# Kernel tuning notes

Hardware: AMD Instinct MI355X
Metric: run time of the kernel (lower is better)

Reference implementation:

```python
import jax, jax.numpy as jnp
import numpy as np

B, S, D, H, FF = 2, 2048, 1024, 16, 4096
HD = D // H
EPS = 1e-5


def _ln(x, g, b):
    m = jnp.mean(x, axis=-1, keepdims=True)
    v = jnp.mean((x - m) ** 2, axis=-1, keepdims=True)
    return (x - m) * jax.lax.rsqrt(v + EPS) * g + b


def _rope(x, cos, sin):
    # non-standard RoPE: split full d_model at half, rotate (pre head-split)
    half = x.shape[-1] // 2
    x1, x2 = x[..., :half], x[..., half:]
    return jnp.concatenate([x1 * cos - x2 * sin, x1 * sin + x2 * cos], axis=-1)


def _heads(x, b, s):
    return x.reshape(b, s, H, HD).transpose(0, 2, 1, 3)  # [b,h,s,hd]


def _attn(q, k, v):
    scores = jnp.einsum('bhqd,bhkd->bhqk', q, k) / jnp.sqrt(jnp.float32(HD))
    w = jax.nn.softmax(scores, axis=-1)
    return jnp.einsum('bhqk,bhkd->bhqd', w, v)


def setup_inputs() -> dict:
    key = jax.random.key(0)
    ks = jax.random.split(key, 32)
    sc = 0.02
    d = {
        'x': jax.random.normal(ks[0], (B, S, D), jnp.float32),
        'cond_emb': jax.random.normal(ks[1], (B, D), jnp.float32),
    }
    # proper RoPE tables over half_dim = D//2
    pos = np.arange(S)[:, None]
    inv = 1.0 / (10000.0 ** (np.arange(D // 2) / (D // 2)))
    ang = pos * inv[None, :]
    d['cos_pos'] = jnp.asarray(np.cos(ang), jnp.float32)
    d['sin_pos'] = jnp.asarray(np.sin(ang), jnp.float32)
    names = ['Wq', 'Wk', 'Wv', 'Wo', 'Wqc', 'Wkc', 'Wvc', 'Woc']
    for i, n in enumerate(names):
        d[n] = jax.random.normal(ks[2 + i], (D, D), jnp.float32) * sc
        d['b' + n[1:]] = jnp.zeros((D,), jnp.float32)
    d['W1'] = jax.random.normal(ks[12], (D, FF), jnp.float32) * sc
    d['b1'] = jnp.zeros((FF,), jnp.float32)
    d['W2'] = jax.random.normal(ks[13], (FF, D), jnp.float32) * sc
    d['b2'] = jnp.zeros((D,), jnp.float32)
    for i in (1, 2, 3):
        d[f'g{i}'] = jnp.ones((D,), jnp.float32)
        d[f'be{i}'] = jnp.zeros((D,), jnp.float32)
    return d


def reference(x, cond_emb, cos_pos, sin_pos,
              Wq, bq, Wk, bk, Wv, bv, Wo, bo,
              Wqc, bqc, Wkc, bkc, Wvc, bvc, Woc, boc,
              W1, b1, W2, b2, g1, be1, g2, be2, g3, be3):
    b, s, _ = x.shape
    # self-attention with RoPE applied on full d_model before head split
    residual = x
    xn = _ln(x, g1, be1)
    q = _rope(xn @ Wq + bq, cos_pos, sin_pos)
    k = _rope(xn @ Wk + bk, cos_pos, sin_pos)
    v = xn @ Wv + bv
    o = _attn(_heads(q, b, s), _heads(k, b, s), _heads(v, b, s))
    o = o.transpose(0, 2, 1, 3).reshape(b, s, D) @ Wo + bo
    x = residual + o
    # cross-attention with single-token context
    residual = x
    xn = _ln(x, g2, be2)
    cond = cond_emb[:, None, :]  # [b,1,D]
    qc = _heads(xn @ Wqc + bqc, b, s)
    kc = _heads(cond @ Wkc + bkc, b, 1)
    vc = _heads(cond @ Wvc + bvc, b, 1)
    oc = _attn(qc, kc, vc)
    oc = oc.transpose(0, 2, 1, 3).reshape(b, s, D) @ Woc + boc
    x = residual + oc
    # FFN (exact GELU)
    residual = x
    xn = _ln(x, g3, be3)
    h = jax.nn.gelu(xn @ W1 + b1, approximate=False)
    return residual + (h @ W2 + b2)
```

## Files before the change

### kernel.cpp

```cpp
#include <hip/hip_runtime.h>
#include <cmath>

#define B_  2
#define S_  2048
#define D_  1024
#define H_  16
#define HD_ 64
#define FF_ 4096
#define M_  4096

typedef __attribute__((ext_vector_type(8))) __bf16 bf16x8;
typedef __attribute__((ext_vector_type(4))) __bf16 bf16x4;
typedef __attribute__((ext_vector_type(4))) float  f32x4;

__device__ __forceinline__ void gload_lds16(void* lds, const void* g) {
    __builtin_amdgcn_global_load_lds(
        (const __attribute__((address_space(1))) unsigned int*)g,
        (__attribute__((address_space(3))) unsigned int*)lds,
        16, 0, 0);
}

#define FENCE() asm volatile("" ::: "memory")

__global__ __launch_bounds__(256)
void tcast(const float* __restrict__ src, __bf16* __restrict__ dst, int K, int N)
{
    __shared__ float t[32][33];
    int tx = threadIdx.x & 31, ty = threadIdx.x >> 5;
    int k0 = blockIdx.y * 32, n0 = blockIdx.x * 32;
#pragma unroll
    for (int i = 0; i < 4; ++i)
        t[ty + i * 8][tx] = src[(size_t)(k0 + ty + i * 8) * N + n0 + tx];
    __syncthreads();
#pragma unroll
    for (int i = 0; i < 4; ++i)
        dst[(size_t)(n0 + ty + i * 8) * K + k0 + tx] = (__bf16)t[tx][ty + i * 8];
}

__global__ __launch_bounds__(256)
void tcast3(const float* __restrict__ wa, const float* __restrict__ wb,
            const float* __restrict__ wc, __bf16* __restrict__ dstb)
{
    __shared__ float t[32][33];
    const float* src = blockIdx.z == 0 ? wa : (blockIdx.z == 1 ? wb : wc);
    __bf16* dst = dstb + (size_t)blockIdx.z * 1024 * 1024;
    int tx = threadIdx.x & 31, ty = threadIdx.x >> 5;
    int k0 = blockIdx.y * 32, n0 = blockIdx.x * 32;
#pragma unroll
    for (int i = 0; i < 4; ++i)
        t[ty + i * 8][tx] = src[(size_t)(k0 + ty + i * 8) * 1024 + n0 + tx];
    __syncthreads();
#pragma unroll
    for (int i = 0; i < 4; ++i)
        dst[(size_t)(n0 + ty + i * 8) * 1024 + k0 + tx] = (__bf16)t[tx][ty + i * 8];
}

__global__ __launch_bounds__(256)
void catb(const float* __restrict__ a, const float* __restrict__ b,
          const float* __restrict__ c, float* __restrict__ o)
{
    int i = blockIdx.x * 256 + threadIdx.x;
    o[i] = i < 1024 ? a[i] : (i < 2048 ? b[i - 1024] : c[i - 2048]);
}

__global__ __launch_bounds__(256)
void colgemv(const float* __restrict__ inp, const float* __restrict__ W,
             const float* __restrict__ bias, float* __restrict__ out, int K, int N)
{
    __shared__ float part[4][16];
    const int b = blockIdx.y;
    const int t = threadIdx.x;
    const int w = t >> 6, lane = t & 63;
    const int colIdx = lane & 15;
    const int col = blockIdx.x * 16 + colIdx;
    const int ks = w * 4 + (lane >> 4);
    const int kpt = K >> 4;
    const float* ip = inp + (size_t)b * K + ks * kpt;
    const float* wp = W + (size_t)ks * kpt * N + col;
    float acc = 0.f;
#pragma unroll 8
    for (int i = 0; i < kpt; ++i)
        acc += ip[i] * wp[(size_t)i * N];
    acc += __shfl_xor(acc, 16);
    acc += __shfl_xor(acc, 32);
    if (lane < 16) part[w][colIdx] = acc;
    __syncthreads();
    if (t < 16) {
        float r = part[0][t] + part[1][t] + part[2][t] + part[3][t]
                + bias[blockIdx.x * 16 + t];
        out[(size_t)b * N + blockIdx.x * 16 + t] = r;
    }
}

__global__ __launch_bounds__(256)
void ln_cast(const float* __restrict__ x, const float* __restrict__ g,
             const float* __restrict__ be, __bf16* __restrict__ out)
{
    int row = blockIdx.x, tid = threadIdx.x;
    const float4* xp = (const float4*)(x + (size_t)row * D_);
    float4 v = xp[tid];
    float s  = v.x + v.y + v.z + v.w;
    float s2 = v.x * v.x + v.y * v.y + v.z * v.z + v.w * v.w;
#pragma unroll
    for (int off = 32; off > 0; off >>= 1) {
        s  += __shfl_down(s, off);
        s2 += __shfl_down(s2, off);
    }
    __shared__ float rs[4], rs2[4];
    int wid = tid >> 6, lane = tid & 63;
    if (lane == 0) { rs[wid] = s; rs2[wid] = s2; }
    __syncthreads();
    float tot  = rs[0] + rs[1] + rs[2] + rs[3];
    float tot2 = rs2[0] + rs2[1] + rs2[2] + rs2[3];
    float mean = tot * (1.0f / D_);
    float var  = tot2 * (1.0f / D_) - mean * mean;
    float rstd = rsqrtf(var + 1e-5f);
    float4 gv = ((const float4*)g)[tid];
    float4 bv = ((const float4*)be)[tid];
    bf16x4 ov;
    ov[0] = (__bf16)((v.x - mean) * rstd * gv.x + bv.x);
    ov[1] = (__bf16)((v.y - mean) * rstd * gv.y + bv.y);
    ov[2] = (__bf16)((v.z - mean) * rstd * gv.z + bv.z);
    ov[3] = (__bf16)((v.w - mean) * rstd * gv.w + bv.w);
    ((bf16x4*)(out + (size_t)row * D_))[tid] = ov;
}

__global__ __launch_bounds__(128)
void rope_qk(const __bf16* __restrict__ qkv, const float* __restrict__ cosp,
             const float* __restrict__ sinp, __bf16* __restrict__ Qh,
             __bf16* __restrict__ Kh)
{
    int row = blockIdx.x, tid = threadIdx.x;
    int b = row >> 11, s = row & 2047;
    float4 c  = ((const float4*)(cosp + (size_t)s * 512))[tid];
    float4 sn = ((const float4*)(sinp + (size_t)s * 512))[tid];
    int d0 = tid * 4;
    int h1 = d0 >> 6, dd = d0 & 63;
#pragma unroll
    for (int which = 0; which < 2; ++which) {
        const int off = which * 1024;
        const float scale = which ? 1.0f : 0.18033688f;
        __bf16* out = which ? Kh : Qh;
        bf16x4 a  = *(const bf16x4*)(qkv + (size_t)row * 3072 + off + tid * 4);
        bf16x4 bb = *(const bf16x4*)(qkv + (size_t)row * 3072 + off + 512 + tid * 4);
        float x1a = (float)a[0],  x1b = (float)a[1],  x1c = (float)a[2],  x1d = (float)a[3];
        float x2a = (float)bb[0], x2b = (float)bb[1], x2c = (float)bb[2], x2d = (float)bb[3];
        bf16x4 o1, o2;
        o1[0] = (__bf16)((x1a * c.x - x2a * sn.x) * scale);
        o1[1] = (__bf16)((x1b * c.y - x2b * sn.y) * scale);
        o1[2] = (__bf16)((x1c * c.z - x2c * sn.z) * scale);
        o1[3] = (__bf16)((x1d * c.w - x2d * sn.w) * scale);
        o2[0] = (__bf16)((x1a * sn.x + x2a * c.x) * scale);
        o2[1] = (__bf16)((x1b * sn.y + x2b * c.y) * scale);
        o2[2] = (__bf16)((x1c * sn.z + x2c * c.z) * scale);
        o2[3] = (__bf16)((x1d * sn.w + x2d * c.w) * scale);
        *(bf16x4*)(out + ((size_t)((b * H_ + h1) * S_ + s) * HD_) + dd) = o1;
        *(bf16x4*)(out + ((size_t)((b * H_ + h1 + 8) * S_ + s) * HD_) + dd) = o2;
    }
}

__global__ __launch_bounds__(256)
void vtrans2(const __bf16* __restrict__ qkv, __bf16* __restrict__ Vt)
{
    __shared__ __bf16 t[32][33];
    int tx = threadIdx.x & 31, ty = threadIdx.x >> 5;
    int bh = blockIdx.z;
    int b = bh >> 4, h = bh & 15;
    int s0 = blockIdx.y * 32, d0 = blockIdx.x * 32;
    __bf16* dst = Vt + (size_t)bh * HD_ * S_;
#pragma unroll
    for (int i = 0; i < 4; ++i)
        t[ty + i * 8][tx] = qkv[(size_t)(b * 2048 + s0 + ty + i * 8) * 3072
                                + 2048 + h * 64 + d0 + tx];
    __syncthreads();
#pragma unroll
    for (int i = 0; i < 4; ++i)
        dst[(size_t)(d0 + ty + i * 8) * S_ + s0 + tx] = t[tx][ty + i * 8];
}

template<int EPI>
__global__ __launch_bounds__(512)
void gemm8(const __bf16* __restrict__ A, const __bf16* __restrict__ Bt,
           const float* __restrict__ bias, __bf16* __restrict__ o0,
           __bf16* __restrict__ o1, int M, int N, int K, int klen)
{
    __shared__ __align__(16) char smem[131072];
    const int tid = threadIdx.x;
    const int wid = tid >> 6, lane = tid & 63;
    const int l15 = lane & 15, l16 = lane >> 4;
    const int wm = wid >> 2, wn = wid & 3;

    const int gx = gridDim.x;
    const int nwg = gx * gridDim.y;
    int wg = blockIdx.y * gx + blockIdx.x;
    wg = (wg & 7) * (nwg >> 3) + (wg >> 3);
    const int n0 = (wg % gx) * 256;
    const int m0 = (wg / gx) * 256;
    const int kz = blockIdx.z * klen;
    const size_t K2 = (size_t)K * 2;

    const int srow = tid >> 3;
    const int scol = ((tid & 7) * 16) ^ ((srow & 7) << 4);
    const char* gA = (const char*)A + (size_t)(m0 + srow) * K2 + (size_t)kz * 2 + scol;
    const char* gB = (const char*)Bt + (size_t)(n0 + srow) * K2 + (size_t)kz * 2 + scol;

    auto stageA = [&](int c) {
        char* d = (char*)smem + c * 32768 + wid * 1024;
        gload_lds16(d,         gA);
        gload_lds16(d + 8192,  gA + 64 * K2);
        gload_lds16(d + 16384, gA + 128 * K2);
        gload_lds16(d + 24576, gA + 192 * K2);
    };
    auto stageB = [&](int c) {
        char* d = (char*)smem + 65536 + c * 32768 + wid * 1024;
        gload_lds16(d,         gB);
        gload_lds16(d + 8192,  gB + 64 * K2);
        gload_lds16(d + 16384, gB + 128 * K2);
        gload_lds16(d + 24576, gB + 192 * K2);
    };

    const int sw = (l15 & 7) << 4;
    const int x0 = (l16 * 16) ^ sw;
    const int x1 = (64 + l16 * 16) ^ sw;
    const int aoff = (wm * 128 + l15) * 128;
    const int boff = 65536 + (wn * 64 + l15) * 128;

    f32x4 acc[8][4] = {};
    const int NT = klen >> 6;

    stageA(0); stageB(0); gA += 128; gB += 128;
    stageA(1); stageB(1); gA += 128; gB += 128;
    asm volatile("s_waitcnt vmcnt(8)" ::: "memory");
    __builtin_amdgcn_s_barrier();

    for (int t = 0; t < NT; ++t) {
        const int cur = t & 1;
        const char* sa = (const char*)smem + cur * 32768;
        const bool pf = (t + 2) < NT;

        bf16x8 af0[8], af1[8];
        bf16x8 b00, b01, b02, b03, b10, b11, b12, b13;

#pragma unroll
        for (int mi = 0; mi < 8; ++mi)
            af0[mi] = *(const bf16x8*)(sa + aoff + mi * 2048 + x0);
        b00 = *(const bf16x8*)(sa + boff + 0 * 2048 + x0);
        b01 = *(const bf16x8*)(sa + boff + 1 * 2048 + x0);
        FENCE();
        __builtin_amdgcn_s_barrier();
        __builtin_amdgcn_s_setprio(1);
#pragma unroll
        for (int mi = 0; mi < 8; ++mi) {
            acc[mi][0] = __builtin_amdgcn_mfma_f32_16x16x32_bf16(af0[mi], b00, acc[mi][0], 0, 0, 0);
            acc[mi][1] = __builtin_amdgcn_mfma_f32_16x16x32_bf16(af0[mi], b01, acc[mi][1], 0, 0, 0);
        }
        __builtin_amdgcn_s_setprio(0);

#pragma unroll
        for (int mi = 0; mi < 8; ++mi)
            af1[mi] = *(const bf16x8*)(sa + aoff + mi * 2048 + x1);
        b02 = *(const bf16x8*)(sa + boff + 2 * 2048 + x0);
        b03 = *(const bf16x8*)(sa + boff + 3 * 2048 + x0);
        FENCE();
        __builtin_amdgcn_s_barrier();
        __builtin_amdgcn_s_setprio(1);
#pragma unroll
        for (int mi = 0; mi < 8; ++mi) {
            acc[mi][2] = __builtin_amdgcn_mfma_f32_16x16x32_bf16(af0[mi], b02, acc[mi][2], 0, 0, 0);
            acc[mi][3] = __builtin_amdgcn_mfma_f32_16x16x32_bf16(af0[mi], b03, acc[mi][3], 0, 0, 0);
        }
        __builtin_amdgcn_s_setprio(0);

        b10 = *(const bf16x8*)(sa + boff + 0 * 2048 + x1);
        b11 = *(const bf16x8*)(sa + boff + 1 * 2048 + x1);
        FENCE();
        __builtin_amdgcn_s_barrier();
        if (pf) stageA(cur);
        __builtin_amdgcn_s_setprio(1);
#pragma unroll
        for (int mi = 0; mi < 8; ++mi) {
            acc[mi][0] = __builtin_amdgcn_mfma_f32_16x16x32_bf16(af1[mi], b10, acc[mi][0], 0, 0, 0);
            acc[mi][1] = __builtin_amdgcn_mfma_f32_16x16x32_bf16(af1[mi], b11, acc[mi][1], 0, 0, 0);
        }
        __builtin_amdgcn_s_setprio(0);

        b12 = *(const bf16x8*)(sa + boff + 2 * 2048 + x1);
        b13 = *(const bf16x8*)(sa + boff + 3 * 2048 + x1);
        FENCE();
        __builtin_amdgcn_s_barrier();
        if (pf) { stageB(cur); gA += 128; gB += 128; }
        __builtin_amdgcn_s_setprio(1);
#pragma unroll
        for (int mi = 0; mi < 8; ++mi) {
            acc[mi][2] = __builtin_amdgcn_mfma_f32_16x16x32_bf16(af1[mi], b12, acc[mi][2], 0, 0, 0);
            acc[mi][3] = __builtin_amdgcn_mfma_f32_16x16x32_bf16(af1[mi], b13, acc[mi][3], 0, 0, 0);
        }
        __builtin_amdgcn_s_setprio(0);
        if (pf) asm volatile("s_waitcnt vmcnt(8)" ::: "memory");
        else    asm volatile("s_waitcnt vmcnt(0)" ::: "memory");
        __builtin_amdgcn_s_barrier();
        FENCE();
    }

#pragma unroll
    for (int mi = 0; mi < 8; ++mi)
#pragma unroll
        for (int ni = 0; ni < 4; ++ni) {
            int gc = n0 + wn * 64 + ni * 16 + l15;
            float bb = (EPI == 2) ? 0.f : bias[gc];
#pragma unroll
            for (int r = 0; r < 4; ++r) {
                int gr = m0 + wm * 128 + mi * 16 + l16 * 4 + r;
                float v = acc[mi][ni][r] + bb;
                if constexpr (EPI == 0) {
                    o0[(size_t)gr * N + gc] = (__bf16)v;
                } else if constexpr (EPI == 1) {
                    o0[(size_t)gr * N + gc] =
                        (__bf16)(0.5f * v * (1.0f + erff(v * 0.70710678118f)));
                } else {
                    const size_t PSZ = (size_t)M_ * 1024;
                    __bf16* po = (blockIdx.z < 2) ? (o0 + blockIdx.z * PSZ)
                                                  : (o1 + (blockIdx.z - 2) * PSZ);
                    po[(size_t)gr * N + gc] = (__bf16)v;
                }
            }
        }
}

__global__ __launch_bounds__(256)
void ffn2_red(const __bf16* __restrict__ pA, const __bf16* __restrict__ pB,
              const float* __restrict__ x2, const float* __restrict__ b2,
              float* __restrict__ out)
{
    const size_t PSZ = (size_t)M_ * 1024;
    size_t i = ((size_t)blockIdx.x * 256 + threadIdx.x) * 8;
    bf16x8 a0 = *(const bf16x8*)(pA + i);
    bf16x8 a1 = *(const bf16x8*)(pA + PSZ + i);
    bf16x8 c0 = *(const bf16x8*)(pB + i);
    bf16x8 c1 = *(const bf16x8*)(pB + PSZ + i);
    float4 xa = *(const float4*)(x2 + i);
    float4 xb = *(const float4*)(x2 + i + 4);
    float xs[8] = {xa.x, xa.y, xa.z, xa.w, xb.x, xb.y, xb.z, xb.w};
#pragma unroll
    for (int j = 0; j < 8; ++j) {
        int col = (int)((i + j) & 1023);
        out[i + j] = xs[j] + b2[col]
                   + (float)a0[j] + (float)a1[j] + (float)c0[j] + (float)c1[j];
    }
}

__global__ __launch_bounds__(256)
void gemm_bt(const __bf16* __restrict__ A, const __bf16* __restrict__ Bt,
             const float* __restrict__ bias, const float* __restrict__ resid,
             const float* __restrict__ extra, float* __restrict__ outF,
             int M, int N, int K)
{
    __shared__ __align__(16) __bf16 As[128 * 64];
    __shared__ __align__(16) __bf16 Bs[128 * 64];
    const int tid = threadIdx.x;
    const int wid = tid >> 6, lane = tid & 63;
    const int m0 = blockIdx.y * 128, n0 = blockIdx.x * 128;
    const int wm = wid >> 1, wn = wid & 1;
    const int l15 = lane & 15, l16 = lane >> 4;

    f32x4 acc[4][4] = {};
    char* asb = (char*)As;
    char* bsb = (char*)Bs;
    const char* ag = (const char*)A;
    const char* bg = (const char*)Bt;
    const int srow = lane >> 3;
    const int scolsw = ((lane & 7) * 16) ^ (srow << 4);

    for (int k0 = 0; k0 < K; k0 += 64) {
        __syncthreads();
#pragma unroll
        for (int i = 0; i < 4; ++i) {
            int j = wid * 4 + i;
            int row = j * 8 + srow;
            gload_lds16(asb + j * 1024,
                        ag + (size_t)(m0 + row) * (K * 2) + k0 * 2 + scolsw);
        }
#pragma unroll
        for (int i = 0; i < 4; ++i) {
            int j = wid * 4 + i;
            int row = j * 8 + srow;
            gload_lds16(bsb + j * 1024,
                        bg + (size_t)(n0 + row) * (K * 2) + k0 * 2 + scolsw);
        }
        __syncthreads();

        bf16x8 af[4][2], bfr[4][2];
#pragma unroll
        for (int mi = 0; mi < 4; ++mi) {
            int row = wm * 64 + mi * 16 + l15;
            int swl = (row & 7) << 4;
#pragma unroll
            for (int kk = 0; kk < 2; ++kk)
                af[mi][kk] = *(const bf16x8*)(asb + row * 128 + ((l16 * 16 + kk * 64) ^ swl));
        }
#pragma unroll
        for (int ni = 0; ni < 4; ++ni) {
            int row = wn * 64 + ni * 16 + l15;
            int swl = (row & 7) << 4;
#pragma unroll
            for (int kk = 0; kk < 2; ++kk)
                bfr[ni][kk] = *(const bf16x8*)(bsb + row * 128 + ((l16 * 16 + kk * 64) ^ swl));
        }
#pragma unroll
        for (int mi = 0; mi < 4; ++mi)
#pragma unroll
            for (int ni = 0; ni < 4; ++ni) {
                acc[mi][ni] = __builtin_amdgcn_mfma_f32_16x16x32_bf16(af[mi][0], bfr[ni][0], acc[mi][ni], 0, 0, 0);
                acc[mi][ni] = __builtin_amdgcn_mfma_f32_16x16x32_bf16(af[mi][1], bfr[ni][1], acc[mi][ni], 0, 0, 0);
            }
    }

#pragma unroll
    for (int mi = 0; mi < 4; ++mi)
#pragma unroll
        for (int ni = 0; ni < 4; ++ni) {
            int gc = n0 + wn * 64 + ni * 16 + l15;
            float bb = bias[gc];
#pragma unroll
            for (int r = 0; r < 4; ++r) {
                int gr = m0 + wm * 64 + mi * 16 + l16 * 4 + r;
                float v = acc[mi][ni][r] + bb;
                size_t idx = (size_t)gr * N + gc;
                int b = gr >> 11;
                outF[idx] = resid[idx] + v + extra[(size_t)b * N + gc];
            }
        }
}

__global__ __launch_bounds__(512)
void attn_fwd(const __bf16* __restrict__ Qh, const __bf16* __restrict__ Kh,
              const __bf16* __restrict__ Vt, __bf16* __restrict__ Op,
              float* __restrict__ Lp)
{
    __shared__ __align__(16) char smem[49152];
    const int tid = threadIdx.x, wid = tid >> 6, lane = tid & 63;
    const int l15 = lane & 15, l16 = lane >> 4;

    const int wg = blockIdx.x;
    const int rr = wg >> 3;
    const int qb = rr & 15;
    const int split = (rr >> 4) & 1;
    const int bh = (wg & 7) + 8 * (rr >> 5);
    const int kt0 = split * 16;

    const int q0 = qb * 128 + wid * 16;
    const size_t qkbase = (size_t)bh * S_ * HD_;

    bf16x8 qf[2];
    {
        const __bf16* qp = Qh + qkbase + (size_t)(q0 + l15) * HD_ + l16 * 8;
        qf[0] = *(const bf16x8*)qp;
        qf[1] = *(const bf16x8*)(qp + 32);
    }
    f32x4 o[4] = {};
    f32x4 accs = {};
    bf16x8 ones;
#pragma unroll
    for (int j = 0; j < 8; ++j) ones[j] = (__bf16)1.0f;

    const int srow = lane >> 3;
    const int scolsw = ((lane & 7) * 16) ^ ((srow & 7) << 4);
    const char* kg = (const char*)(Kh + qkbase);
    const char* vg = (const char*)(Vt + (size_t)bh * HD_ * S_);

    auto stage = [&](int c, int t) {
        int s0 = t * 64;
        int row = wid * 8 + srow;
        gload_lds16(smem + c * 8192 + wid * 1024,
                    kg + (size_t)(s0 + row) * 128 + scolsw);
        gload_lds16(smem + 16384 + c * 8192 + wid * 1024,
                    vg + (size_t)row * (S_ * 2) + s0 * 2 + scolsw);
    };

    const int NT = 16;
    stage(0, kt0);
    stage(1, kt0 + 1);
    asm volatile("s_waitcnt vmcnt(2)" ::: "memory");
    __builtin_amdgcn_s_barrier();

    for (int ki = 0; ki < NT; ++ki) {
        const int cur = ki & 1;
        const char* Kl = smem + cur * 8192;
        const char* Vl = smem + 16384 + cur * 8192;
        char* Pl = smem + 32768 + wid * 2048;

        f32x4 st[4];
        __builtin_amdgcn_s_setprio(1);
#pragma unroll
        for (int t = 0; t < 4; ++t) {
            int row = t * 16 + l15;
            int swl = (row & 7) << 4;
            bf16x8 ak0 = *(const bf16x8*)(Kl + row * 128 + ((l16 * 16) ^ swl));
            bf16x8 ak1 = *(const bf16x8*)(Kl + row * 128 + ((l16 * 16 + 64) ^ swl));
            f32x4 z = {0.f, 0.f, 0.f, 0.f};
            z = __builtin_amdgcn_mfma_f32_16x16x32_bf16(ak0, qf[0], z, 0, 0, 0);
            st[t] = __builtin_amdgcn_mfma_f32_16x16x32_bf16(ak1, qf[1], z, 0, 0, 0);
        }
        __builtin_amdgcn_s_setprio(0);

        float p[4][4];
#pragma unroll
        for (int t = 0; t < 4; ++t)
#pragma unroll
            for (int r = 0; r < 4; ++r) p[t][r] = exp2f(st[t][r]);

        {
            char* pw = Pl + l15 * 128;
            int swl = (l15 & 7) << 4;
#pragma unroll
            for (int t = 0; t < 4; ++t) {
                bf16x4 pk;
                pk[0] = (__bf16)p[t][0]; pk[1] = (__bf16)p[t][1];
                pk[2] = (__bf16)p[t][2]; pk[3] = (__bf16)p[t][3];
                *(bf16x4*)(pw + ((t * 32 + l16 * 8) ^ swl)) = pk;
            }
        }
        {
            const char* pr = Pl + l15 * 128;
            int swp = (l15 & 7) << 4;
            bf16x8 ap0 = *(const bf16x8*)(pr + ((l16 * 16) ^ swp));
            bf16x8 ap1 = *(const bf16x8*)(pr + ((l16 * 16 + 64) ^ swp));
            __builtin_amdgcn_s_setprio(1);
            accs = __builtin_amdgcn_mfma_f32_16x16x32_bf16(ap0, ones, accs, 0, 0, 0);
            accs = __builtin_amdgcn_mfma_f32_16x16x32_bf16(ap1, ones, accs, 0, 0, 0);
#pragma unroll
            for (int dg = 0; dg < 4; ++dg) {
                int row = dg * 16 + l15;
                int swl = (row & 7) << 4;
                bf16x8 bv0 = *(const bf16x8*)(Vl + row * 128 + ((l16 * 16) ^ swl));
                bf16x8 bv1 = *(const bf16x8*)(Vl + row * 128 + ((l16 * 16 + 64) ^ swl));
                o[dg] = __builtin_amdgcn_mfma_f32_16x16x32_bf16(ap0, bv0, o[dg], 0, 0, 0);
                o[dg] = __builtin_amdgcn_mfma_f32_16x16x32_bf16(ap1, bv1, o[dg], 0, 0, 0);
            }
            __builtin_amdgcn_s_setprio(0);
        }

        FENCE();
        __builtin_amdgcn_s_barrier();
        if (ki + 2 < NT) {
            stage(cur, kt0 + ki + 2);
            asm volatile("s_waitcnt vmcnt(2)" ::: "memory");
        } else {
            asm volatile("s_waitcnt vmcnt(0)" ::: "memory");
        }
        __builtin_amdgcn_s_barrier();
        FENCE();
    }

    __bf16* ob = Op + ((size_t)split * 65536 + (size_t)bh * 2048) * 64;
#pragma unroll
    for (int r = 0; r < 4; ++r) {
        float inv = 1.0f / accs[r];
        int qg = q0 + l16 * 4 + r;
#pragma unroll
        for (int dg = 0; dg < 4; ++dg)
            ob[(size_t)qg * 64 + dg * 16 + l15] = (__bf16)(o[dg][r] * inv);
    }
    if (l15 == 0) {
#pragma unroll
        for (int r = 0; r < 4; ++r)
            Lp[(size_t)split * 65536 + (size_t)bh * 2048 + q0 + l16 * 4 + r]
                = log2f(accs[r]);
    }
}

__global__ __launch_bounds__(256)
void attn_merge(const __bf16* __restrict__ Op, const float* __restrict__ Lp,
                __bf16* __restrict__ O)
{
    int idx = blockIdx.x * 256 + threadIdx.x;
    int bh = idx >> 14;
    int rem = idx & 16383;
    int s = rem >> 3;
    int d0 = (rem & 7) * 8;
    size_t qi = (size_t)bh * 2048 + s;
    float L1 = Lp[qi], L2 = Lp[65536 + qi];
    float Lm = fmaxf(L1, L2);
    float w1 = exp2f(L1 - Lm), w2 = exp2f(L2 - Lm);
    float inv = 1.0f / (w1 + w2);
    w1 *= inv; w2 *= inv;
    bf16x8 o1 = *(const bf16x8*)(Op + qi * 64 + d0);
    bf16x8 o2 = *(const bf16x8*)(Op + (size_t)65536 * 64 + qi * 64 + d0);
    int b = bh >> 4, h = bh & 15;
    __bf16* op = O + ((size_t)(b * S_ + s) * D_) + h * 64 + d0;
    bf16x8 ov;
#pragma unroll
    for (int j = 0; j < 8; ++j)
        ov[j] = (__bf16)(w1 * (float)o1[j] + w2 * (float)o2[j]);
    *(bf16x8*)op = ov;
}

extern "C" void kernel_launch(void* const* d_in, const int* in_sizes, int n_in,
                              void* d_out, int out_size, void* d_ws, size_t ws_size,
                              hipStream_t stream)
{
    (void)in_sizes; (void)n_in; (void)out_size; (void)ws_size;
    const float* x    = (const float*)d_in[0];
    const float* cond = (const float*)d_in[1];
    const float* cosp = (const float*)d_in[2];
    const float* sinp = (const float*)d_in[3];
    const float* Wq = (const float*)d_in[4];  const float* bq = (const float*)d_in[5];
    const float* Wk = (const float*)d_in[6];  const float* bk = (const float*)d_in[7];
    const float* Wv = (const float*)d_in[8];  const float* bv = (const float*)d_in[9];
    const float* Wo = (const float*)d_in[10]; const float* bo = (const float*)d_in[11];
    const float* Wvc = (const float*)d_in[16]; const float* bvc = (const float*)d_in[17];
    const float* Woc = (const float*)d_in[18]; const float* boc = (const float*)d_in[19];
    const float* W1 = (const float*)d_in[20]; const float* b1 = (const float*)d_in[21];
    const float* W2 = (const float*)d_in[22]; const float* b2 = (const float*)d_in[23];
    const float* g1 = (const float*)d_in[24]; const float* be1 = (const float*)d_in[25];
    const float* g3 = (const float*)d_in[28]; const float* be3 = (const float*)d_in[29];

    char* ws = (char*)d_ws;
    const size_t MB = 1ull << 20;
    __bf16* WqkvT = (__bf16*)(ws + 0 * MB);
    __bf16* WoT   = (__bf16*)(ws + 6 * MB);
    __bf16* W1T   = (__bf16*)(ws + 8 * MB);
    __bf16* W2T   = (__bf16*)(ws + 16 * MB);
    __bf16* xn    = (__bf16*)(ws + 24 * MB);
    __bf16* qkvh  = (__bf16*)(ws + 32 * MB);
    __bf16* Qh    = (__bf16*)(ws + 56 * MB);
    __bf16* Kh    = (__bf16*)(ws + 64 * MB);
    __bf16* Vt    = (__bf16*)(ws + 72 * MB);
    __bf16* oflat = (__bf16*)(ws + 80 * MB);
    float*  bqkv  = (float*)(ws + 88 * MB);
    float*  vc    = (float*)(ws + 88 * MB + 16384);
    float*  ocp   = (float*)(ws + 88 * MB + 32768);
    __bf16* Opart = (__bf16*)(ws + 32 * MB);
    float*  Lpart = (float*)(ws + 48 * MB);
    float*  x2    = (float*)(ws + 32 * MB);
    __bf16* hbuf  = (__bf16*)(ws + 48 * MB);
    __bf16* pA    = (__bf16*)(ws + 0 * MB);
    __bf16* pB    = (__bf16*)(ws + 80 * MB);

    tcast3<<<dim3(32, 32, 3), 256, 0, stream>>>(Wq, Wk, Wv, WqkvT);
    tcast<<<dim3(32, 32),  256, 0, stream>>>(Wo, WoT, 1024, 1024);
    tcast<<<dim3(128, 32), 256, 0, stream>>>(W1, W1T, 1024, 4096);
    tcast<<<dim3(32, 128), 256, 0, stream>>>(W2, W2T, 4096, 1024);
    catb<<<12, 256, 0, stream>>>(bq, bk, bv, bqkv);
    colgemv<<<dim3(64, 2), 256, 0, stream>>>(cond, Wvc, bvc, vc, 1024, 1024);
    colgemv<<<dim3(64, 2), 256, 0, stream>>>(vc, Woc, boc, ocp, 1024, 1024);
    ln_cast<<<M_, 256, 0, stream>>>(x, g1, be1, xn);
    gemm8<0><<<dim3(12, 16, 1), 512, 0, stream>>>(xn, WqkvT, bqkv, qkvh, nullptr,
                                                  M_, 3072, 1024, 1024);
    rope_qk<<<M_, 128, 0, stream>>>(qkvh, cosp, sinp, Qh, Kh);
    vtrans2<<<dim3(2, 64, 32), 256, 0, stream>>>(qkvh, Vt);
    attn_fwd<<<1024, 512, 0, stream>>>(Qh, Kh, Vt, Opart, Lpart);
    attn_merge<<<2048, 256, 0, stream>>>(Opart, Lpart, oflat);
    gemm_bt<<<dim3(8, 32), 256, 0, stream>>>(oflat, WoT, bo, x, ocp, x2,
                                             M_, 1024, 1024);
    ln_cast<<<M_, 256, 0, stream>>>(x2, g3, be3, xn);
    gemm8<1><<<dim3(16, 16, 1), 512, 0, stream>>>(xn, W1T, b1, hbuf, nullptr,
                                                  M_, 4096, 1024, 1024);
    gemm8<2><<<dim3(4, 16, 4), 512, 0, stream>>>(hbuf, W2T, nullptr, pA, pB,
                                                 M_, 1024, 4096, 1024);
    ffn2_red<<<2048, 256, 0, stream>>>(pA, pB, x2, b2, (float*)d_out);
}
```

Baseline: 268.2 us.

## Merge weight-cast and rope/V-transpose launches; drop split-K attention merge

Folds the four weight transpose-cast kernels and the bias concat into one launch, and folds RoPE and the V transpose into one launch. Attention no longer splits the key range in two. Each workgroup now walks all 32 key tiles and writes normalized output straight into the flat head-interleaved layout, which removes the partial-output buffers and the merge kernel. The aim is to cut launch overhead and partial-result traffic. The cost is that attention now runs 512 workgroups of 512 threads instead of 1024, which may leave compute units underfilled.

```diff
diff --git a/kernel.cpp b/kernel.cpp
--- a/kernel.cpp
+++ b/kernel.cpp
@@ -23,44 +23,44 @@
 #define FENCE() asm volatile("" ::: "memory")
 
 __global__ __launch_bounds__(256)
-void tcast(const float* __restrict__ src, __bf16* __restrict__ dst, int K, int N)
-{
-    __shared__ float t[32][33];
+void tcastall(const float* __restrict__ Wq, const float* __restrict__ Wk,
+              const float* __restrict__ Wv, const float* __restrict__ Wo,
+              const float* __restrict__ W1, const float* __restrict__ W2,
+              __bf16* __restrict__ WqkvT, __bf16* __restrict__ WoT,
+              __bf16* __restrict__ W1T, __bf16* __restrict__ W2T,
+              const float* __restrict__ bq, const float* __restrict__ bk,
+              const float* __restrict__ bv, float* __restrict__ bqkv)
+{
+    const int id = blockIdx.x;
+    if (id >= 12288) {
+        int i = (id - 12288) * 256 + threadIdx.x;
+        bqkv[i] = i < 1024 ? bq[i] : (i < 2048 ? bk[i - 1024] : bv[i - 2048]);
+        return;
+    }
+    const float* src; __bf16* dst; int K, N, t, lg;
+    if (id < 3072) {
+        int w = id >> 10;
+        src = w == 0 ? Wq : (w == 1 ? Wk : Wv);
+        dst = WqkvT + (size_t)w * 1024 * 1024;
+        K = 1024; N = 1024; t = id & 1023; lg = 5;
+    } else if (id < 4096) {
+        src = Wo; dst = WoT; K = 1024; N = 1024; t = id - 3072; lg = 5;
+    } else if (id < 8192) {
+        src = W1; dst = W1T; K = 1024; N = 4096; t = id - 4096; lg = 7;
+    } else {
+        src = W2; dst = W2T; K = 4096; N = 1024; t = id - 8192; lg = 5;
+    }
+    const int bx = t & ((1 << lg) - 1), by = t >> lg;
+    const int k0 = by * 32, n0 = bx * 32;
+    __shared__ float tb[32][33];
     int tx = threadIdx.x & 31, ty = threadIdx.x >> 5;
-    int k0 = blockIdx.y * 32, n0 = blockIdx.x * 32;
 #pragma unroll
     for (int i = 0; i < 4; ++i)
-        t[ty + i * 8][tx] = src[(size_t)(k0 + ty + i * 8) * N + n0 + tx];
+        tb[ty + i * 8][tx] = src[(size_t)(k0 + ty + i * 8) * N + n0 + tx];
     __syncthreads();
 #pragma unroll
     for (int i = 0; i < 4; ++i)
-        dst[(size_t)(n0 + ty + i * 8) * K + k0 + tx] = (__bf16)t[tx][ty + i * 8];
-}
-
-__global__ __launch_bounds__(256)
-void tcast3(const float* __restrict__ wa, const float* __restrict__ wb,
-            const float* __restrict__ wc, __bf16* __restrict__ dstb)
-{
-    __shared__ float t[32][33];
-    const float* src = blockIdx.z == 0 ? wa : (blockIdx.z == 1 ? wb : wc);
-    __bf16* dst = dstb + (size_t)blockIdx.z * 1024 * 1024;
-    int tx = threadIdx.x & 31, ty = threadIdx.x >> 5;
-    int k0 = blockIdx.y * 32, n0 = blockIdx.x * 32;
-#pragma unroll
-    for (int i = 0; i < 4; ++i)
-        t[ty + i * 8][tx] = src[(size_t)(k0 + ty + i * 8) * 1024 + n0 + tx];
-    __syncthreads();
-#pragma unroll
-    for (int i = 0; i < 4; ++i)
-        dst[(size_t)(n0 + ty + i * 8) * 1024 + k0 + tx] = (__bf16)t[tx][ty + i * 8];
-}
-
-__global__ __launch_bounds__(256)
-void catb(const float* __restrict__ a, const float* __restrict__ b,
-          const float* __restrict__ c, float* __restrict__ o)
-{
-    int i = blockIdx.x * 256 + threadIdx.x;
-    o[i] = i < 1024 ? a[i] : (i < 2048 ? b[i - 1024] : c[i - 2048]);
+        dst[(size_t)(n0 + ty + i * 8) * K + k0 + tx] = (__bf16)tb[tx][ty + i * 8];
 }
 
 __global__ __launch_bounds__(256)
@@ -125,48 +125,48 @@
     ((bf16x4*)(out + (size_t)row * D_))[tid] = ov;
 }
 
-__global__ __launch_bounds__(128)
-void rope_qk(const __bf16* __restrict__ qkv, const float* __restrict__ cosp,
-             const float* __restrict__ sinp, __bf16* __restrict__ Qh,
-             __bf16* __restrict__ Kh)
-{
-    int row = blockIdx.x, tid = threadIdx.x;
-    int b = row >> 11, s = row & 2047;
-    float4 c  = ((const float4*)(cosp + (size_t)s * 512))[tid];
-    float4 sn = ((const float4*)(sinp + (size_t)s * 512))[tid];
-    int d0 = tid * 4;
-    int h1 = d0 >> 6, dd = d0 & 63;
-#pragma unroll
-    for (int which = 0; which < 2; ++which) {
-        const int off = which * 1024;
-        const float scale = which ? 1.0f : 0.18033688f;
-        __bf16* out = which ? Kh : Qh;
-        bf16x4 a  = *(const bf16x4*)(qkv + (size_t)row * 3072 + off + tid * 4);
-        bf16x4 bb = *(const bf16x4*)(qkv + (size_t)row * 3072 + off + 512 + tid * 4);
-        float x1a = (float)a[0],  x1b = (float)a[1],  x1c = (float)a[2],  x1d = (float)a[3];
-        float x2a = (float)bb[0], x2b = (float)bb[1], x2c = (float)bb[2], x2d = (float)bb[3];
-        bf16x4 o1, o2;
-        o1[0] = (__bf16)((x1a * c.x - x2a * sn.x) * scale);
-        o1[1] = (__bf16)((x1b * c.y - x2b * sn.y) * scale);
-        o1[2] = (__bf16)((x1c * c.z - x2c * sn.z) * scale);
-        o1[3] = (__bf16)((x1d * c.w - x2d * sn.w) * scale);
-        o2[0] = (__bf16)((x1a * sn.x + x2a * c.x) * scale);
-        o2[1] = (__bf16)((x1b * sn.y + x2b * c.y) * scale);
-        o2[2] = (__bf16)((x1c * sn.z + x2c * c.z) * scale);
-        o2[3] = (__bf16)((x1d * sn.w + x2d * c.w) * scale);
-        *(bf16x4*)(out + ((size_t)((b * H_ + h1) * S_ + s) * HD_) + dd) = o1;
-        *(bf16x4*)(out + ((size_t)((b * H_ + h1 + 8) * S_ + s) * HD_) + dd) = o2;
-    }
-}
-
 __global__ __launch_bounds__(256)
-void vtrans2(const __bf16* __restrict__ qkv, __bf16* __restrict__ Vt)
-{
+void ropev(const __bf16* __restrict__ qkv, const float* __restrict__ cosp,
+           const float* __restrict__ sinp, __bf16* __restrict__ Qh,
+           __bf16* __restrict__ Kh, __bf16* __restrict__ Vt)
+{
+    const int id = blockIdx.x;
     __shared__ __bf16 t[32][33];
+    if (id < 2048) {
+        int row = id * 2 + (threadIdx.x >> 7);
+        int tid = threadIdx.x & 127;
+        int b = row >> 11, s = row & 2047;
+        float4 c  = ((const float4*)(cosp + (size_t)s * 512))[tid];
+        float4 sn = ((const float4*)(sinp + (size_t)s * 512))[tid];
+        int d0 = tid * 4;
+        int h1 = d0 >> 6, dd = d0 & 63;
+#pragma unroll
+        for (int which = 0; which < 2; ++which) {
+            const int off = which * 1024;
+            const float scale = which ? 1.0f : 0.18033688f;
+            __bf16* out = which ? Kh : Qh;
+            bf16x4 a  = *(const bf16x4*)(qkv + (size_t)row * 3072 + off + tid * 4);
+            bf16x4 bb = *(const bf16x4*)(qkv + (size_t)row * 3072 + off + 512 + tid * 4);
+            float x1a = (float)a[0],  x1b = (float)a[1],  x1c = (float)a[2],  x1d = (float)a[3];
+            float x2a = (float)bb[0], x2b = (float)bb[1], x2c = (float)bb[2], x2d = (float)bb[3];
+            bf16x4 o1, o2;
+            o1[0] = (__bf16)((x1a * c.x - x2a * sn.x) * scale);
+            o1[1] = (__bf16)((x1b * c.y - x2b * sn.y) * scale);
+            o1[2] = (__bf16)((x1c * c.z - x2c * sn.z) * scale);
+            o1[3] = (__bf16)((x1d * c.w - x2d * sn.w) * scale);
+            o2[0] = (__bf16)((x1a * sn.x + x2a * c.x) * scale);
+            o2[1] = (__bf16)((x1b * sn.y + x2b * c.y) * scale);
+            o2[2] = (__bf16)((x1c * sn.z + x2c * c.z) * scale);
+            o2[3] = (__bf16)((x1d * sn.w + x2d * c.w) * scale);
+            *(bf16x4*)(out + ((size_t)((b * H_ + h1) * S_ + s) * HD_) + dd) = o1;
+            *(bf16x4*)(out + ((size_t)((b * H_ + h1 + 8) * S_ + s) * HD_) + dd) = o2;
+        }
+        return;
+    }
+    int v = id - 2048;
+    int d0 = (v & 1) * 32, s0 = ((v >> 1) & 63) * 32, bh = v >> 7;
+    int b = bh >> 4, h = bh & 15;
     int tx = threadIdx.x & 31, ty = threadIdx.x >> 5;
-    int bh = blockIdx.z;
-    int b = bh >> 4, h = bh & 15;
-    int s0 = blockIdx.y * 32, d0 = blockIdx.x * 32;
     __bf16* dst = Vt + (size_t)bh * HD_ * S_;
 #pragma unroll
     for (int i = 0; i < 4; ++i)
@@ -434,8 +434,7 @@
 
 __global__ __launch_bounds__(512)
 void attn_fwd(const __bf16* __restrict__ Qh, const __bf16* __restrict__ Kh,
-              const __bf16* __restrict__ Vt, __bf16* __restrict__ Op,
-              float* __restrict__ Lp)
+              const __bf16* __restrict__ Vt, __bf16* __restrict__ O)
 {
     __shared__ __align__(16) char smem[49152];
     const int tid = threadIdx.x, wid = tid >> 6, lane = tid & 63;
@@ -444,9 +443,7 @@
     const int wg = blockIdx.x;
     const int rr = wg >> 3;
     const int qb = rr & 15;
-    const int split = (rr >> 4) & 1;
-    const int bh = (wg & 7) + 8 * (rr >> 5);
-    const int kt0 = split * 16;
+    const int bh = (wg & 7) + 8 * (rr >> 4);
 
     const int q0 = qb * 128 + wid * 16;
     const size_t qkbase = (size_t)bh * S_ * HD_;
@@ -477,9 +474,9 @@
                     vg + (size_t)row * (S_ * 2) + s0 * 2 + scolsw);
     };
 
-    const int NT = 16;
-    stage(0, kt0);
-    stage(1, kt0 + 1);
+    const int NT = S_ / 64;
+    stage(0, 0);
+    stage(1, 1);
     asm volatile("s_waitcnt vmcnt(2)" ::: "memory");
     __builtin_amdgcn_s_barrier();
 
@@ -543,7 +540,7 @@
         FENCE();
         __builtin_amdgcn_s_barrier();
         if (ki + 2 < NT) {
-            stage(cur, kt0 + ki + 2);
+            stage(cur, ki + 2);
             asm volatile("s_waitcnt vmcnt(2)" ::: "memory");
         } else {
             asm volatile("s_waitcnt vmcnt(0)" ::: "memory");
@@ -552,47 +549,16 @@
         FENCE();
     }
 
-    __bf16* ob = Op + ((size_t)split * 65536 + (size_t)bh * 2048) * 64;
+    int b = bh >> 4, hh = bh & 15;
 #pragma unroll
     for (int r = 0; r < 4; ++r) {
         float inv = 1.0f / accs[r];
         int qg = q0 + l16 * 4 + r;
+        __bf16* op = O + ((size_t)(b * S_ + qg) * D_) + hh * HD_;
 #pragma unroll
         for (int dg = 0; dg < 4; ++dg)
-            ob[(size_t)qg * 64 + dg * 16 + l15] = (__bf16)(o[dg][r] * inv);
-    }
-    if (l15 == 0) {
-#pragma unroll
-        for (int r = 0; r < 4; ++r)
-            Lp[(size_t)split * 65536 + (size_t)bh * 2048 + q0 + l16 * 4 + r]
-                = log2f(accs[r]);
-    }
-}
-
-__global__ __launch_bounds__(256)
-void attn_merge(const __bf16* __restrict__ Op, const float* __restrict__ Lp,
-                __bf16* __restrict__ O)
-{
-    int idx = blockIdx.x * 256 + threadIdx.x;
-    int bh = idx >> 14;
-    int rem = idx & 16383;
-    int s = rem >> 3;
-    int d0 = (rem & 7) * 8;
-    size_t qi = (size_t)bh * 2048 + s;
-    float L1 = Lp[qi], L2 = Lp[65536 + qi];
-    float Lm = fmaxf(L1, L2);
-    float w1 = exp2f(L1 - Lm), w2 = exp2f(L2 - Lm);
-    float inv = 1.0f / (w1 + w2);
-    w1 *= inv; w2 *= inv;
-    bf16x8 o1 = *(const bf16x8*)(Op + qi * 64 + d0);
-    bf16x8 o2 = *(const bf16x8*)(Op + (size_t)65536 * 64 + qi * 64 + d0);
-    int b = bh >> 4, h = bh & 15;
-    __bf16* op = O + ((size_t)(b * S_ + s) * D_) + h * 64 + d0;
-    bf16x8 ov;
-#pragma unroll
-    for (int j = 0; j < 8; ++j)
-        ov[j] = (__bf16)(w1 * (float)o1[j] + w2 * (float)o2[j]);
-    *(bf16x8*)op = ov;
+            op[dg * 16 + l15] = (__bf16)(o[dg][r] * inv);
+    }
 }
 
 extern "C" void kernel_launch(void* const* d_in, const int* in_sizes, int n_in,
@@ -630,27 +596,20 @@
     float*  bqkv  = (float*)(ws + 88 * MB);
     float*  vc    = (float*)(ws + 88 * MB + 16384);
     float*  ocp   = (float*)(ws + 88 * MB + 32768);
-    __bf16* Opart = (__bf16*)(ws + 32 * MB);
-    float*  Lpart = (float*)(ws + 48 * MB);
     float*  x2    = (float*)(ws + 32 * MB);
     __bf16* hbuf  = (__bf16*)(ws + 48 * MB);
     __bf16* pA    = (__bf16*)(ws + 0 * MB);
     __bf16* pB    = (__bf16*)(ws + 80 * MB);
 
-    tcast3<<<dim3(32, 32, 3), 256, 0, stream>>>(Wq, Wk, Wv, WqkvT);
-    tcast<<<dim3(32, 32),  256, 0, stream>>>(Wo, WoT, 1024, 1024);
-    tcast<<<dim3(128, 32), 256, 0, stream>>>(W1, W1T, 1024, 4096);
-    tcast<<<dim3(32, 128), 256, 0, stream>>>(W2, W2T, 4096, 1024);
-    catb<<<12, 256, 0, stream>>>(bq, bk, bv, bqkv);
+    tcastall<<<12300, 256, 0, stream>>>(Wq, Wk, Wv, Wo, W1, W2,
+                                        WqkvT, WoT, W1T, W2T, bq, bk, bv, bqkv);
     colgemv<<<dim3(64, 2), 256, 0, stream>>>(cond, Wvc, bvc, vc, 1024, 1024);
     colgemv<<<dim3(64, 2), 256, 0, stream>>>(vc, Woc, boc, ocp, 1024, 1024);
     ln_cast<<<M_, 256, 0, stream>>>(x, g1, be1, xn);
     gemm8<0><<<dim3(12, 16, 1), 512, 0, stream>>>(xn, WqkvT, bqkv, qkvh, nullptr,
                                                   M_, 3072, 1024, 1024);
-    rope_qk<<<M_, 128, 0, stream>>>(qkvh, cosp, sinp, Qh, Kh);
-    vtrans2<<<dim3(2, 64, 32), 256, 0, stream>>>(qkvh, Vt);
-    attn_fwd<<<1024, 512, 0, stream>>>(Qh, Kh, Vt, Opart, Lpart);
-    attn_merge<<<2048, 256, 0, stream>>>(Opart, Lpart, oflat);
+    ropev<<<6144, 256, 0, stream>>>(qkvh, cosp, sinp, Qh, Kh, Vt);
+    attn_fwd<<<512, 512, 0, stream>>>(Qh, Kh, Vt, oflat);
     gemm_bt<<<dim3(8, 32), 256, 0, stream>>>(oflat, WoT, bo, x, ocp, x2,
                                              M_, 1024, 1024);
     ln_cast<<<M_, 256, 0, stream>>>(x2, g3, be3, xn);
```

Result: faster. 253.5 us (-5.5%).
